# Optimization experiments

Hardware: AMD Instinct MI355X
Metric: run time of the kernel (lower is better)

The kernel has to match this reference:

```python
import jax, jax.numpy as jnp
import numpy as np

N, F_IN = 50000, 128      # nodes, input channels
H, C = 4, 32              # attention heads, out channels per head (concat -> H*C = 128)
E = 800000                # directed edges (before self loops)
NEG_SLOPE = 0.2
EPS = 1e-5                # GraphNorm eps


def setup_inputs() -> dict:
    key = jax.random.key(0)
    ks = jax.random.split(key, 9)
    s = 1.0 / np.sqrt(F_IN)
    return {
        "x": jax.random.normal(ks[0], (N, F_IN), jnp.float32),
        "edge_index": jax.random.randint(ks[1], (2, E), 0, N, jnp.int32),
        "W_l": jax.random.uniform(ks[2], (F_IN, H * C), jnp.float32, -s, s),  # source proj
        "W_r": jax.random.uniform(ks[3], (F_IN, H * C), jnp.float32, -s, s),  # target proj
        "att": jax.random.uniform(ks[4], (H, C), jnp.float32, -s, s),         # GATv2 attention vector a
        "bias": jnp.zeros((H * C,), jnp.float32),
        "gn_weight": jnp.ones((H * C,), jnp.float32),
        "gn_bias": jnp.zeros((H * C,), jnp.float32),
        "gn_mean_scale": jnp.ones((H * C,), jnp.float32),
    }


def _gatv2_graphnorm(x, edge_index, W_l, W_r, att, bias, gn_weight, gn_bias, gn_mean_scale):
    n = x.shape[0]
    # add self loops (add_self_loops=True)
    ar = jnp.arange(n, dtype=edge_index.dtype)
    src = jnp.concatenate([edge_index[0], ar])  # message source j
    dst = jnp.concatenate([edge_index[1], ar])  # message target i

    x_l = (x @ W_l).reshape(n, H, C)  # source-side features
    x_r = (x @ W_r).reshape(n, H, C)  # target-side features

    # GATv2 score: a . LeakyReLU(W_l x_j + W_r x_i), per edge per head  [E+N, H]
    e = jax.nn.leaky_relu(x_l[src] + x_r[dst], NEG_SLOPE)
    score = jnp.einsum("ehc,hc->eh", e, att)

    # softmax over each destination's incoming edges (segment softmax)
    smax = jax.ops.segment_max(score, dst, num_segments=n)
    ex = jnp.exp(score - smax[dst])
    denom = jax.ops.segment_sum(ex, dst, num_segments=n)
    alpha = ex / denom[dst]  # [E+N, H]

    # aggregate messages: out_i = sum_j alpha_ij * (W_l x_j)
    out = jax.ops.segment_sum(alpha[:, :, None] * x_l[src], dst, num_segments=n)
    out = out.reshape(n, H * C) + bias  # concat heads

    # GraphNorm (single graph): per-feature mean/var over all nodes
    mean = out.mean(axis=0)
    centered = out - gn_mean_scale * mean
    var = (centered * centered).mean(axis=0)
    return gn_weight * centered * jax.lax.rsqrt(var + EPS) + gn_bias


def reference(x, edge_index, W_l, W_r, att, bias, gn_weight, gn_bias, gn_mean_scale):
    return _gatv2_graphnorm(x, edge_index, W_l, W_r, att, bias, gn_weight, gn_bias, gn_mean_scale)
```

## Files before the change

### kernel.cpp

```cpp
#include <hip/hip_runtime.h>
#include <hip/hip_bf16.h>
#include <math.h>

#define N_NODES 50000
#define F_IN 128
#define HC 128
#define N_EDGES 800000
#define E_TOT (N_EDGES + N_NODES)
#define NEG_SLOPE 0.2f
#define GN_EPS 1e-5f
#define DEG_STRIDE 16
#define CAP 64
#define EB ((E_TOT + 255) / 256)
#define GB ((N_NODES + 63) / 64)

typedef __attribute__((ext_vector_type(8))) short short8;
typedef __attribute__((ext_vector_type(4))) float floatx4;

__device__ inline ushort f2bf(float f) {
    unsigned u = __float_as_uint(f);
    u += 0x7FFF + ((u >> 16) & 1);
    return (ushort)(u >> 16);
}

__global__ __launch_bounds__(256) void wprep_k(const float* __restrict__ Wl,
                                               const float* __restrict__ Wr,
                                               ushort* __restrict__ wtl,
                                               ushort* __restrict__ wtr) {
    int i = blockIdx.x * 256 + threadIdx.x;
    int k = i >> 7, n = i & 127;
    wtl[n * 128 + k] = f2bf(Wl[i]);
    wtr[n * 128 + k] = f2bf(Wr[i]);
}

__global__ __launch_bounds__(256) void edge_k(const int* __restrict__ ei,
                                              int* __restrict__ deg16,
                                              int* __restrict__ csr_pad) {
    int e = blockIdx.x * 256 + threadIdx.x;
    if (e >= E_TOT) return;
    int src, dst;
    if (e < N_EDGES) { src = ei[e]; dst = ei[N_EDGES + e]; }
    else             { src = dst = e - N_EDGES; }
    int r = atomicAdd(&deg16[dst * DEG_STRIDE], 1);
    if (r < CAP) csr_pad[dst * CAP + r] = src;
}

__global__ __launch_bounds__(256) void gemm2_k(const float* __restrict__ x,
                                               const ushort* __restrict__ wtl,
                                               const ushort* __restrict__ wtr,
                                               ushort* __restrict__ xlb,
                                               ushort* __restrict__ xrb) {
    __shared__ ushort Wt[2][128][136];
    const int tid = threadIdx.x;
#pragma unroll
    for (int i = 0; i < 8; ++i) {
        int n = i * 16 + (tid >> 4);
        int k8 = (tid & 15) * 8;
        *(int4*)&Wt[0][n][k8] = *(const int4*)(wtl + n * 128 + k8);
        *(int4*)&Wt[1][n][k8] = *(const int4*)(wtr + n * 128 + k8);
    }
    __syncthreads();

    const int w = tid >> 6, lane = tid & 63;
    const int quad = lane >> 4, l16 = lane & 15;
    const int rbase = blockIdx.x * 64 + w * 16;
    const int grow = rbase + l16;
    const float* ap = x + (size_t)(grow < N_NODES ? grow : (N_NODES - 1)) * F_IN + quad * 8;

    floatx4 accL[8], accR[8];
#pragma unroll
    for (int nt = 0; nt < 8; ++nt) {
        accL[nt] = (floatx4){0.f, 0.f, 0.f, 0.f};
        accR[nt] = (floatx4){0.f, 0.f, 0.f, 0.f};
    }

#pragma unroll
    for (int ks = 0; ks < 4; ++ks) {
        float4 a0 = *(const float4*)(ap + ks * 32 + 0);
        float4 a1 = *(const float4*)(ap + ks * 32 + 4);
        short8 af;
        af[0] = (short)f2bf(a0.x); af[1] = (short)f2bf(a0.y);
        af[2] = (short)f2bf(a0.z); af[3] = (short)f2bf(a0.w);
        af[4] = (short)f2bf(a1.x); af[5] = (short)f2bf(a1.y);
        af[6] = (short)f2bf(a1.z); af[7] = (short)f2bf(a1.w);
#pragma unroll
        for (int nt = 0; nt < 8; ++nt) {
            short8 bfl = *(const short8*)&Wt[0][nt * 16 + l16][ks * 32 + quad * 8];
            short8 bfr = *(const short8*)&Wt[1][nt * 16 + l16][ks * 32 + quad * 8];
            accL[nt] = __builtin_amdgcn_mfma_f32_16x16x32_bf16(af, bfl, accL[nt], 0, 0, 0);
            accR[nt] = __builtin_amdgcn_mfma_f32_16x16x32_bf16(af, bfr, accR[nt], 0, 0, 0);
        }
    }
#pragma unroll
    for (int r = 0; r < 4; ++r) {
        int gro = rbase + quad * 4 + r;
        if (gro < N_NODES) {
            ushort* opl = xlb + (size_t)gro * HC + l16;
            ushort* opr = xrb + (size_t)gro * HC + l16;
#pragma unroll
            for (int nt = 0; nt < 8; ++nt) {
                opl[nt * 16] = f2bf(accL[nt][r]);
                opr[nt * 16] = f2bf(accR[nt][r]);
            }
        }
    }
}

__global__ __launch_bounds__(256) void attn_k(const ushort* __restrict__ xlb,
                                              const ushort* __restrict__ xrb,
                                              const int* __restrict__ deg16,
                                              const int* __restrict__ csr_pad,
                                              const float* __restrict__ att,
                                              const float* __restrict__ bias,
                                              float* __restrict__ out) {
    const int wid = threadIdx.x >> 6, lane = threadIdx.x & 63;
    const int dst = blockIdx.x * 4 + wid;
    if (dst >= N_NODES) return;
    const int e = lane >> 4, s = lane & 15;
    float xrv[8], av[8];
    {
        int4 xv = *(const int4*)(xrb + (size_t)dst * HC + s * 8);
        xrv[0] = __uint_as_float(((unsigned)xv.x) << 16);
        xrv[1] = __uint_as_float(((unsigned)xv.x) & 0xffff0000u);
        xrv[2] = __uint_as_float(((unsigned)xv.y) << 16);
        xrv[3] = __uint_as_float(((unsigned)xv.y) & 0xffff0000u);
        xrv[4] = __uint_as_float(((unsigned)xv.z) << 16);
        xrv[5] = __uint_as_float(((unsigned)xv.z) & 0xffff0000u);
        xrv[6] = __uint_as_float(((unsigned)xv.w) << 16);
        xrv[7] = __uint_as_float(((unsigned)xv.w) & 0xffff0000u);
        float4 a0 = *(const float4*)(att + s * 8);
        float4 a1 = *(const float4*)(att + s * 8 + 4);
        av[0] = a0.x; av[1] = a0.y; av[2] = a0.z; av[3] = a0.w;
        av[4] = a1.x; av[5] = a1.y; av[6] = a1.z; av[7] = a1.w;
    }
    float l = 0.f;
    float acc[8] = {0.f, 0.f, 0.f, 0.f, 0.f, 0.f, 0.f, 0.f};
    const int nk = min(deg16[dst * DEG_STRIDE], CAP);
    const int sv = csr_pad[dst * CAP + lane];

#define EDGE_STEP(rv, valid)                                                   \
    {                                                                          \
        float f0 = __uint_as_float(((unsigned)(rv).x) << 16);                  \
        float f1 = __uint_as_float(((unsigned)(rv).x) & 0xffff0000u);          \
        float f2 = __uint_as_float(((unsigned)(rv).y) << 16);                  \
        float f3 = __uint_as_float(((unsigned)(rv).y) & 0xffff0000u);          \
        float f4 = __uint_as_float(((unsigned)(rv).z) << 16);                  \
        float f5 = __uint_as_float(((unsigned)(rv).z) & 0xffff0000u);          \
        float f6 = __uint_as_float(((unsigned)(rv).w) << 16);                  \
        float f7 = __uint_as_float(((unsigned)(rv).w) & 0xffff0000u);          \
        float t, part;                                                         \
        t = f0 + xrv[0]; t = t > 0.f ? t : NEG_SLOPE * t; part = av[0] * t;    \
        t = f1 + xrv[1]; t = t > 0.f ? t : NEG_SLOPE * t; part += av[1] * t;   \
        t = f2 + xrv[2]; t = t > 0.f ? t : NEG_SLOPE * t; part += av[2] * t;   \
        t = f3 + xrv[3]; t = t > 0.f ? t : NEG_SLOPE * t; part += av[3] * t;   \
        t = f4 + xrv[4]; t = t > 0.f ? t : NEG_SLOPE * t; part += av[4] * t;   \
        t = f5 + xrv[5]; t = t > 0.f ? t : NEG_SLOPE * t; part += av[5] * t;   \
        t = f6 + xrv[6]; t = t > 0.f ? t : NEG_SLOPE * t; part += av[6] * t;   \
        t = f7 + xrv[7]; t = t > 0.f ? t : NEG_SLOPE * t; part += av[7] * t;   \
        part += __shfl_xor(part, 1, 4);                                        \
        part += __shfl_xor(part, 2, 4);                                        \
        float p = (valid) ? __expf(part) : 0.f;                                \
        l += p;                                                                \
        acc[0] += p * f0; acc[1] += p * f1; acc[2] += p * f2; acc[3] += p * f3;\
        acc[4] += p * f4; acc[5] += p * f5; acc[6] += p * f6; acc[7] += p * f7;\
    }

    int j = 0;
    for (; j + 8 <= nk; j += 8) {
        int s0 = __shfl(sv, j + e, 64);
        int s1 = __shfl(sv, j + 4 + e, 64);
        int4 r0 = *(const int4*)(xlb + (size_t)s0 * HC + s * 8);
        int4 r1 = *(const int4*)(xlb + (size_t)s1 * HC + s * 8);
        EDGE_STEP(r0, true);
        EDGE_STEP(r1, true);
    }
    for (; j < nk; j += 4) {
        int idx = j + e;
        bool valid = idx < nk;
        int s0 = __shfl(sv, valid ? idx : 0, 64);
        int4 r0 = *(const int4*)(xlb + (size_t)s0 * HC + s * 8);
        EDGE_STEP(r0, valid);
    }
#undef EDGE_STEP

    l += __shfl_xor(l, 16, 64);
    l += __shfl_xor(l, 32, 64);
#pragma unroll
    for (int c = 0; c < 8; ++c) {
        acc[c] += __shfl_xor(acc[c], 16, 64);
        acc[c] += __shfl_xor(acc[c], 32, 64);
    }
    if (e == 0) {
        float inv = 1.0f / l;
        float4 b0 = *(const float4*)(bias + s * 8);
        float4 b1 = *(const float4*)(bias + s * 8 + 4);
        float4 o0 = make_float4(acc[0] * inv + b0.x, acc[1] * inv + b0.y,
                                acc[2] * inv + b0.z, acc[3] * inv + b0.w);
        float4 o1 = make_float4(acc[4] * inv + b1.x, acc[5] * inv + b1.y,
                                acc[6] * inv + b1.z, acc[7] * inv + b1.w);
        *(float4*)(out + (size_t)dst * HC + s * 8)     = o0;
        *(float4*)(out + (size_t)dst * HC + s * 8 + 4) = o1;
    }
}

__global__ __launch_bounds__(256) void stats_k(const float* __restrict__ out,
                                               float* __restrict__ gsum,
                                               float* __restrict__ gsumsq) {
    int f = threadIdx.x & 127;
    int half = threadIdx.x >> 7;
    float s = 0.f, s2 = 0.f;
    for (int r = blockIdx.x * 2 + half; r < N_NODES; r += gridDim.x * 2) {
        float v = out[(size_t)r * HC + f];
        s += v; s2 += v * v;
    }
    __shared__ float l1[256], l2[256];
    l1[threadIdx.x] = s; l2[threadIdx.x] = s2;
    __syncthreads();
    if (threadIdx.x < 128) {
        s  = l1[threadIdx.x] + l1[threadIdx.x + 128];
        s2 = l2[threadIdx.x] + l2[threadIdx.x + 128];
        atomicAdd(&gsum[f], s);
        atomicAdd(&gsumsq[f], s2);
    }
}

__global__ __launch_bounds__(256) void norm_k(float* __restrict__ out,
                                              const float* __restrict__ gsum,
                                              const float* __restrict__ gsumsq,
                                              const float* __restrict__ gw,
                                              const float* __restrict__ gb,
                                              const float* __restrict__ gms) {
    int f = threadIdx.x & 127;
    int half = threadIdx.x >> 7;
    const float invN = 1.0f / (float)N_NODES;
    float mean = gsum[f] * invN;
    float msq  = gsumsq[f] * invN;
    float g = gms[f];
    float var = msq - 2.f * g * mean * mean + g * g * mean * mean;
    float rstd = rsqrtf(var + GN_EPS);
    float a = gw[f] * rstd;
    float b = gb[f] - a * g * mean;
    for (int r = blockIdx.x * 2 + half; r < N_NODES; r += gridDim.x * 2) {
        size_t o = (size_t)r * HC + f;
        out[o] = a * out[o] + b;
    }
}

extern "C" void kernel_launch(void* const* d_in, const int* in_sizes, int n_in,
                              void* d_out, int out_size, void* d_ws, size_t ws_size,
                              hipStream_t stream) {
    const float* x    = (const float*)d_in[0];
    const int*   ei   = (const int*)d_in[1];
    const float* Wl   = (const float*)d_in[2];
    const float* Wr   = (const float*)d_in[3];
    const float* att  = (const float*)d_in[4];
    const float* bias = (const float*)d_in[5];
    const float* gw   = (const float*)d_in[6];
    const float* gb   = (const float*)d_in[7];
    const float* gms  = (const float*)d_in[8];
    float* out = (float*)d_out;

    ushort* xlb   = (ushort*)d_ws;
    ushort* xrb   = xlb + (size_t)N_NODES * HC;
    float*  gsum   = (float*)(xrb + (size_t)N_NODES * HC);
    float*  gsumsq = gsum + HC;
    int*    deg16  = (int*)(gsumsq + HC);
    size_t  zero_bytes = (size_t)(HC + HC) * 4 + (size_t)N_NODES * DEG_STRIDE * 4;
    int*    csr_pad = deg16 + (size_t)N_NODES * DEG_STRIDE;
    ushort* wtl     = (ushort*)(csr_pad + (size_t)N_NODES * CAP);
    ushort* wtr     = wtl + 16384;

    hipMemsetAsync((void*)gsum, 0, zero_bytes, stream);
    hipLaunchKernelGGL(wprep_k, dim3(64), dim3(256), 0, stream,
                       Wl, Wr, wtl, wtr);
    hipLaunchKernelGGL(edge_k, dim3(EB), dim3(256), 0, stream,
                       ei, deg16, csr_pad);
    hipLaunchKernelGGL(gemm2_k, dim3(GB), dim3(256), 0, stream,
                       x, wtl, wtr, xlb, xrb);
    hipLaunchKernelGGL(attn_k, dim3(N_NODES / 4), dim3(256), 0, stream,
                       xlb, xrb, deg16, csr_pad, att, bias, out);
    hipLaunchKernelGGL(stats_k, dim3(256), dim3(256), 0, stream,
                       out, gsum, gsumsq);
    hipLaunchKernelGGL(norm_k, dim3(512), dim3(256), 0, stream,
                       out, gsum, gsumsq, gw, gb, gms);
}
```

Before: 239.8 us.

## Fuse weight prep into edge kernel, store CSR as u16, enlarge GEMM blocks

The weight transpose/convert kernel is folded into the edge-bucketing kernel, saving one launch. Each edge thread now handles two edges. The padded CSR neighbour list is stored as 16-bit indices instead of 32-bit, halving its write and read traffic, which is valid because node ids stay below 65536. The GEMM kernel moves to 512-thread blocks covering 128 rows, so the shared-memory weight tile is loaded half as often; the cost is fewer blocks and higher per-block resource use.

After: 236.6 us. Within noise of the previous version (-1.4%).

```diff
diff --git a/kernel.cpp b/kernel.cpp
--- a/kernel.cpp
+++ b/kernel.cpp
@@ -7,12 +7,13 @@
 #define HC 128
 #define N_EDGES 800000
 #define E_TOT (N_EDGES + N_NODES)
+#define E_HALF (E_TOT / 2)
 #define NEG_SLOPE 0.2f
 #define GN_EPS 1e-5f
 #define DEG_STRIDE 16
 #define CAP 64
-#define EB ((E_TOT + 255) / 256)
-#define GB ((N_NODES + 63) / 64)
+#define EB ((E_HALF + 255) / 256)
+#define GB ((N_NODES + 127) / 128)
 
 typedef __attribute__((ext_vector_type(8))) short short8;
 typedef __attribute__((ext_vector_type(4))) float floatx4;
@@ -23,29 +24,36 @@
     return (ushort)(u >> 16);
 }
 
-__global__ __launch_bounds__(256) void wprep_k(const float* __restrict__ Wl,
-                                               const float* __restrict__ Wr,
-                                               ushort* __restrict__ wtl,
-                                               ushort* __restrict__ wtr) {
-    int i = blockIdx.x * 256 + threadIdx.x;
-    int k = i >> 7, n = i & 127;
-    wtl[n * 128 + k] = f2bf(Wl[i]);
-    wtr[n * 128 + k] = f2bf(Wr[i]);
-}
-
 __global__ __launch_bounds__(256) void edge_k(const int* __restrict__ ei,
                                               int* __restrict__ deg16,
-                                              int* __restrict__ csr_pad) {
-    int e = blockIdx.x * 256 + threadIdx.x;
-    if (e >= E_TOT) return;
-    int src, dst;
-    if (e < N_EDGES) { src = ei[e]; dst = ei[N_EDGES + e]; }
-    else             { src = dst = e - N_EDGES; }
-    int r = atomicAdd(&deg16[dst * DEG_STRIDE], 1);
-    if (r < CAP) csr_pad[dst * CAP + r] = src;
-}
-
-__global__ __launch_bounds__(256) void gemm2_k(const float* __restrict__ x,
+                                              ushort* __restrict__ csrp,
+                                              const float* __restrict__ Wl,
+                                              const float* __restrict__ Wr,
+                                              ushort* __restrict__ wtl,
+                                              ushort* __restrict__ wtr) {
+    int gid = blockIdx.x * 256 + threadIdx.x;
+    if (gid < 16384) {
+        int k = gid >> 7, n = gid & 127;
+        wtl[n * 128 + k] = f2bf(Wl[gid]);
+        wtr[n * 128 + k] = f2bf(Wr[gid]);
+    }
+    if (gid >= E_HALF) return;
+    {
+        int src = ei[gid], dst = ei[N_EDGES + gid];
+        int r = atomicAdd(&deg16[dst * DEG_STRIDE], 1);
+        if (r < CAP) csrp[dst * CAP + r] = (ushort)src;
+    }
+    {
+        int e = gid + E_HALF;
+        int src, dst;
+        if (e < N_EDGES) { src = ei[e]; dst = ei[N_EDGES + e]; }
+        else             { src = dst = e - N_EDGES; }
+        int r = atomicAdd(&deg16[dst * DEG_STRIDE], 1);
+        if (r < CAP) csrp[dst * CAP + r] = (ushort)src;
+    }
+}
+
+__global__ __launch_bounds__(512) void gemm2_k(const float* __restrict__ x,
                                                const ushort* __restrict__ wtl,
                                                const ushort* __restrict__ wtr,
                                                ushort* __restrict__ xlb,
@@ -53,9 +61,9 @@
     __shared__ ushort Wt[2][128][136];
     const int tid = threadIdx.x;
 #pragma unroll
-    for (int i = 0; i < 8; ++i) {
-        int n = i * 16 + (tid >> 4);
-        int k8 = (tid & 15) * 8;
+    for (int i = 0; i < 4; ++i) {
+        int idx = i * 512 + tid;
+        int n = idx >> 4, k8 = (idx & 15) * 8;
         *(int4*)&Wt[0][n][k8] = *(const int4*)(wtl + n * 128 + k8);
         *(int4*)&Wt[1][n][k8] = *(const int4*)(wtr + n * 128 + k8);
     }
@@ -63,7 +71,7 @@
 
     const int w = tid >> 6, lane = tid & 63;
     const int quad = lane >> 4, l16 = lane & 15;
-    const int rbase = blockIdx.x * 64 + w * 16;
+    const int rbase = blockIdx.x * 128 + w * 16;
     const int grow = rbase + l16;
     const float* ap = x + (size_t)(grow < N_NODES ? grow : (N_NODES - 1)) * F_IN + quad * 8;
 
@@ -109,7 +117,7 @@
 __global__ __launch_bounds__(256) void attn_k(const ushort* __restrict__ xlb,
                                               const ushort* __restrict__ xrb,
                                               const int* __restrict__ deg16,
-                                              const int* __restrict__ csr_pad,
+                                              const ushort* __restrict__ csrp,
                                               const float* __restrict__ att,
                                               const float* __restrict__ bias,
                                               float* __restrict__ out) {
@@ -136,7 +144,7 @@
     float l = 0.f;
     float acc[8] = {0.f, 0.f, 0.f, 0.f, 0.f, 0.f, 0.f, 0.f};
     const int nk = min(deg16[dst * DEG_STRIDE], CAP);
-    const int sv = csr_pad[dst * CAP + lane];
+    const int sv = (int)csrp[dst * CAP + lane];
 
 #define EDGE_STEP(rv, valid)                                                   \
     {                                                                          \
@@ -266,19 +274,17 @@
     float*  gsumsq = gsum + HC;
     int*    deg16  = (int*)(gsumsq + HC);
     size_t  zero_bytes = (size_t)(HC + HC) * 4 + (size_t)N_NODES * DEG_STRIDE * 4;
-    int*    csr_pad = deg16 + (size_t)N_NODES * DEG_STRIDE;
-    ushort* wtl     = (ushort*)(csr_pad + (size_t)N_NODES * CAP);
-    ushort* wtr     = wtl + 16384;
+    ushort* csrp = (ushort*)(deg16 + (size_t)N_NODES * DEG_STRIDE);
+    ushort* wtl  = csrp + (size_t)N_NODES * CAP;
+    ushort* wtr  = wtl + 16384;
 
     hipMemsetAsync((void*)gsum, 0, zero_bytes, stream);
-    hipLaunchKernelGGL(wprep_k, dim3(64), dim3(256), 0, stream,
-                       Wl, Wr, wtl, wtr);
     hipLaunchKernelGGL(edge_k, dim3(EB), dim3(256), 0, stream,
-                       ei, deg16, csr_pad);
-    hipLaunchKernelGGL(gemm2_k, dim3(GB), dim3(256), 0, stream,
+                       ei, deg16, csrp, Wl, Wr, wtl, wtr);
+    hipLaunchKernelGGL(gemm2_k, dim3(GB), dim3(512), 0, stream,
                        x, wtl, wtr, xlb, xrb);
     hipLaunchKernelGGL(attn_k, dim3(N_NODES / 4), dim3(256), 0, stream,
-                       xlb, xrb, deg16, csr_pad, att, bias, out);
+                       xlb, xrb, deg16, csrp, att, bias, out);
     hipLaunchKernelGGL(stats_k, dim3(256), dim3(256), 0, stream,
                        out, gsum, gsumsq);
     hipLaunchKernelGGL(norm_k, dim3(512), dim3(256), 0, stream,
```
